# Kernel tuning notes

Hardware: AMD Instinct MI355X
Metric: run time of the kernel (lower is better)

Reference implementation:

```python
import jax, jax.numpy as jnp
import numpy as np

N_SITES = 16
BATCH = 8192
K = 256
EPS = 1e-10


def _entanglement_entropy(sites_A, sites_B):
    # sites_A: [b, pA, k], sites_B: [b, pB, k]
    corr = jnp.einsum('bik,bjk->bij', sites_A, sites_B)  # [b, pA, pB]
    s = jnp.linalg.svd(corr, compute_uv=False)           # [b, min(pA,pB)]
    s_sq = s * s + EPS
    p = s_sq / jnp.sum(s_sq, axis=-1, keepdims=True)
    return -jnp.sum(p * jnp.log(p + EPS), axis=-1)        # [b]


def setup_inputs() -> dict:
    key = jax.random.key(0)
    sites = jax.random.normal(key, (BATCH, N_SITES, K), dtype=jnp.float32)
    return {"sites": sites}


def reference(sites) -> jnp.ndarray:
    # sites: [batch, n_sites, k]; list-of-tensors in the original, stacked here.
    n = sites.shape[1]
    mid = n // 2  # 8
    # Whole-system bipartition
    S_whole = _entanglement_entropy(sites[:, :mid], sites[:, mid:])
    # Left half bipartition (mid_left = mid // 2 = 4)
    ml = mid // 2
    S_left = _entanglement_entropy(sites[:, :ml], sites[:, ml:mid])
    # Right half bipartition
    nr = n - mid
    mr = nr // 2
    S_right = _entanglement_entropy(sites[:, mid:mid + mr], sites[:, mid + mr:])
    phi_q = S_whole - (S_left + S_right)
    return jax.nn.relu(phi_q)
```

## Files before the change

### kernel.cpp

```cpp
#include <hip/hip_runtime.h>
#include <math.h>

#define DEV __device__ __forceinline__

typedef float v2f __attribute__((ext_vector_type(2)));

DEV float rcp_fast(float x) { return __builtin_amdgcn_rcpf(x); }
DEV float rsq_fast(float x) { return __builtin_amdgcn_rsqf(x); }

__host__ __device__ constexpr int TI(int n, int i, int j) {
  return n * i - (i * (i - 1)) / 2 + (j - i);
}

template <int N>
DEV float& sym_at(float (&a)[N * (N + 1) / 2], int i, int j) {
  return (i <= j) ? a[TI(N, i, j)] : a[TI(N, j, i)];
}

template <int N>
DEV void pivot_params(float (&a)[N * (N + 1) / 2], int p, int q,
                      float& c_out, float& s_out) {
  float apq = a[TI(N, p, q)];
  float app = a[TI(N, p, p)];
  float aqq = a[TI(N, q, q)];
  float h = aqq - app;
  float tw = apq + apq;
  float den = fabsf(h) + sqrtf(fmaf(h, h, tw * tw)) + 1e-37f;
  float t = tw * rcp_fast(den);
  t = (h < 0.0f) ? -t : t;
  float c = rsq_fast(fmaf(t, t, 1.0f));
  float s = t * c;
  c_out = c;
  s_out = s;
  a[TI(N, p, p)] = fmaf(-t, apq, app);
  a[TI(N, q, q)] = fmaf( t, apq, aqq);
  a[TI(N, p, q)] = 0.0f;
}

template <int N>
DEV void cross_update(float (&a)[N * (N + 1) / 2], int pa, int qa, int pb,
                      int qb, float ca, float sa, float cb, float sb) {
  float w = sym_at<N>(a, pa, pb), x = sym_at<N>(a, pa, qb);
  float y = sym_at<N>(a, qa, pb), z = sym_at<N>(a, qa, qb);
  float w1 = fmaf(ca, w, -sa * y), x1 = fmaf(ca, x, -sa * z);
  float y1 = fmaf(sa, w,  ca * y), z1 = fmaf(sa, x,  ca * z);
  sym_at<N>(a, pa, pb) = fmaf(cb, w1, -sb * x1);
  sym_at<N>(a, pa, qb) = fmaf(sb, w1,  cb * x1);
  sym_at<N>(a, qa, pb) = fmaf(cb, y1, -sb * z1);
  sym_at<N>(a, qa, qb) = fmaf(sb, y1,  cb * z1);
}

template <int SWEEPS>
DEV void pjacobi8(float (&a)[36]) {
  constexpr int P[7][4][2] = {
      {{0, 7}, {1, 6}, {2, 5}, {3, 4}}, {{0, 1}, {2, 7}, {3, 6}, {4, 5}},
      {{0, 2}, {1, 3}, {4, 7}, {5, 6}}, {{0, 3}, {2, 4}, {1, 5}, {6, 7}},
      {{0, 4}, {3, 5}, {2, 6}, {1, 7}}, {{0, 5}, {4, 6}, {3, 7}, {1, 2}},
      {{0, 6}, {5, 7}, {1, 4}, {2, 3}}};
  for (int sw = 0; sw < SWEEPS; ++sw) {
#pragma unroll
    for (int r = 0; r < 7; ++r) {
      float cc[4], ss[4];
#pragma unroll
      for (int u = 0; u < 4; ++u)
        pivot_params<8>(a, P[r][u][0], P[r][u][1], cc[u], ss[u]);
#pragma unroll
      for (int u = 0; u < 4; ++u) {
#pragma unroll
        for (int v = u + 1; v < 4; ++v) {
          cross_update<8>(a, P[r][u][0], P[r][u][1], P[r][v][0], P[r][v][1],
                          cc[u], ss[u], cc[v], ss[v]);
        }
      }
    }
  }
}

template <int SWEEPS>
DEV void pjacobi4x2(float (&a)[10], float (&b)[10]) {
  constexpr int P[3][2][2] = {
      {{0, 3}, {1, 2}}, {{0, 1}, {2, 3}}, {{0, 2}, {1, 3}}};
  for (int sw = 0; sw < SWEEPS; ++sw) {
#pragma unroll
    for (int r = 0; r < 3; ++r) {
      float ca0, sa0, ca1, sa1, cb0, sb0, cb1, sb1;
      pivot_params<4>(a, P[r][0][0], P[r][0][1], ca0, sa0);
      pivot_params<4>(b, P[r][0][0], P[r][0][1], cb0, sb0);
      pivot_params<4>(a, P[r][1][0], P[r][1][1], ca1, sa1);
      pivot_params<4>(b, P[r][1][0], P[r][1][1], cb1, sb1);
      cross_update<4>(a, P[r][0][0], P[r][0][1], P[r][1][0], P[r][1][1], ca0,
                      sa0, ca1, sa1);
      cross_update<4>(b, P[r][0][0], P[r][0][1], P[r][1][0], P[r][1][1], cb0,
                      sb0, cb1, sb1);
    }
  }
}

template <int N>
DEV float entropy_of(const float (&a)[N * (N + 1) / 2]) {
  float lam[N];
  float sum = 0.0f;
#pragma unroll
  for (int i = 0; i < N; ++i) {
    float l = fmaxf(a[TI(N, i, i)], 0.0f) + 1e-10f;
    lam[i] = l;
    sum += l;
  }
  float inv = 1.0f / sum;
  float H = 0.0f;
#pragma unroll
  for (int i = 0; i < N; ++i) {
    float p = lam[i] * inv;
    H = fmaf(p, __logf(p + 1e-10f), H);
  }
  return -H;
}

__global__ __launch_bounds__(256) void corr_kernel(
    const float* __restrict__ sites, float* __restrict__ cmat) {
  const int lane = threadIdx.x & 63;
  const int b = blockIdx.x * 4 + (threadIdx.x >> 6);
  const float4* base = reinterpret_cast<const float4*>(sites) + (size_t)b * 1024;

  v2f lo[16], hi[16];
#pragma unroll
  for (int s = 0; s < 16; ++s) {
    float4 f = base[s * 64 + lane];
    lo[s] = v2f{f.x, f.y};
    hi[s] = v2f{f.z, f.w};
  }

  const int up0 = lane & 1;

  float w[32];
#pragma unroll
  for (int m = 0; m < 32; ++m) {
    const int e0 = 2 * m, e1 = 2 * m + 1;
    const int i0 = e0 >> 3, j0 = e0 & 7;
    const int i1 = e1 >> 3, j1 = e1 & 7;
    v2f t0 = __builtin_elementwise_fma(hi[i0], hi[8 + j0], lo[i0] * lo[8 + j0]);
    v2f t1 = __builtin_elementwise_fma(hi[i1], hi[8 + j1], lo[i1] * lo[8 + j1]);
    float p0 = t0.x + t0.y;
    float p1 = t1.x + t1.y;
    float snd = up0 ? p0 : p1;
    float kp  = up0 ? p1 : p0;
    w[m] = kp + __shfl_xor(snd, 1, 64);
  }
#pragma unroll
  for (int d = 1; d < 6; ++d) {
    const int dist = 1 << d;
    const int up = (lane >> d) & 1;
#pragma unroll
    for (int m = 0; m < (64 >> (d + 1)); ++m) {
      float snd = up ? w[2 * m]     : w[2 * m + 1];
      float kp  = up ? w[2 * m + 1] : w[2 * m];
      w[m] = kp + __shfl_xor(snd, dist, 64);
    }
  }
  float cw = w[0];

  float x[16];
#pragma unroll
  for (int m = 0; m < 16; ++m) {
    const int e0 = 2 * m, e1 = 2 * m + 1;
    const int base_a = (e0 < 16) ? 0 : 8;
    const int ii0 = ((e0 & 15) >> 2), jj0 = (e0 & 3);
    const int ii1 = ((e1 & 15) >> 2), jj1 = (e1 & 3);
    v2f t0 = __builtin_elementwise_fma(hi[base_a + ii0], hi[base_a + 4 + jj0],
                                       lo[base_a + ii0] * lo[base_a + 4 + jj0]);
    v2f t1 = __builtin_elementwise_fma(hi[base_a + ii1], hi[base_a + 4 + jj1],
                                       lo[base_a + ii1] * lo[base_a + 4 + jj1]);
    float p0 = t0.x + t0.y;
    float p1 = t1.x + t1.y;
    float snd = up0 ? p0 : p1;
    float kp  = up0 ? p1 : p0;
    x[m] = kp + __shfl_xor(snd, 1, 64);
  }
#pragma unroll
  for (int d = 1; d < 5; ++d) {
    const int dist = 1 << d;
    const int up = (lane >> d) & 1;
#pragma unroll
    for (int m = 0; m < (32 >> (d + 1)); ++m) {
      float snd = up ? x[2 * m]     : x[2 * m + 1];
      float kp  = up ? x[2 * m + 1] : x[2 * m];
      x[m] = kp + __shfl_xor(snd, dist, 64);
    }
  }
  float clr = x[0] + __shfl_xor(x[0], 32, 64);

  float* row = cmat + (size_t)b * 96;
  row[lane] = cw;
  if (lane < 32) row[64 + lane] = clr;
}

__global__ __launch_bounds__(64) void phi_kernel(
    const float* __restrict__ cmat, float* __restrict__ out) {
  __shared__ float4 lds[64 * 25];
  const int t = threadIdx.x;
  const int b0 = blockIdx.x * 64;

  const float4* src = reinterpret_cast<const float4*>(cmat) + (size_t)b0 * 24;
#pragma unroll
  for (int r = 0; r < 24; ++r) {
    int q = r * 64 + t;
    float4 val = src[q];
    int bl = q / 24;
    int e4 = q - bl * 24;
    lds[bl * 25 + e4] = val;
  }
  __syncthreads();

  const float4* myrow = &lds[t * 25];
  float Cw[64], Cl[16], Cr[16];
#pragma unroll
  for (int j = 0; j < 16; ++j) {
    float4 f = myrow[j];
    Cw[4 * j] = f.x; Cw[4 * j + 1] = f.y; Cw[4 * j + 2] = f.z; Cw[4 * j + 3] = f.w;
  }
#pragma unroll
  for (int j = 0; j < 4; ++j) {
    float4 f = myrow[16 + j];
    Cl[4 * j] = f.x; Cl[4 * j + 1] = f.y; Cl[4 * j + 2] = f.z; Cl[4 * j + 3] = f.w;
    float4 g = myrow[20 + j];
    Cr[4 * j] = g.x; Cr[4 * j + 1] = g.y; Cr[4 * j + 2] = g.z; Cr[4 * j + 3] = g.w;
  }

  float Mw[36];
#pragma unroll
  for (int i = 0; i < 8; ++i) {
#pragma unroll
    for (int j = i; j < 8; ++j) {
      float acc = 0.0f;
#pragma unroll
      for (int k = 0; k < 8; ++k) acc = fmaf(Cw[i * 8 + k], Cw[j * 8 + k], acc);
      Mw[TI(8, i, j)] = acc;
    }
  }
  float Ml[10], Mr[10];
#pragma unroll
  for (int i = 0; i < 4; ++i) {
#pragma unroll
    for (int j = i; j < 4; ++j) {
      float accl = 0.0f, accr = 0.0f;
#pragma unroll
      for (int k = 0; k < 4; ++k) {
        accl = fmaf(Cl[i * 4 + k], Cl[j * 4 + k], accl);
        accr = fmaf(Cr[i * 4 + k], Cr[j * 4 + k], accr);
      }
      Ml[TI(4, i, j)] = accl;
      Mr[TI(4, i, j)] = accr;
    }
  }

  pjacobi8<3>(Mw);
  pjacobi4x2<3>(Ml, Mr);

  float Sw = entropy_of<8>(Mw);
  float Sl = entropy_of<4>(Ml);
  float Sr = entropy_of<4>(Mr);

  out[b0 + t] = fmaxf(Sw - Sl - Sr, 0.0f);
}

extern "C" void kernel_launch(void* const* d_in, const int* in_sizes, int n_in,
                              void* d_out, int out_size, void* d_ws, size_t ws_size,
                              hipStream_t stream) {
  const float* sites = (const float*)d_in[0];
  float* out = (float*)d_out;
  float* cmat = (float*)d_ws;

  corr_kernel<<<2048, 256, 0, stream>>>(sites, cmat);
  phi_kernel<<<128, 64, 0, stream>>>(cmat, out);
}
```

Baseline: 204.3 us.

## Fuse correlation and Jacobi entropy kernels into one launch via LDS

Merges the correlation kernel and the phi/Jacobi kernel into a single kernel. Each block writes its four batch rows of correlation values into shared memory, and then four threads run the Jacobi eigen-solve and entropy for those rows. This removes the workspace round trip through global memory and the second kernel launch. In exchange, the serial Jacobi work now runs on only four threads per 256-thread block while the other threads sit idle, and the same 256-register-class launch bounds now apply to the heavy solver code.

```diff
diff --git a/kernel.cpp b/kernel.cpp
--- a/kernel.cpp
+++ b/kernel.cpp
@@ -116,10 +116,12 @@
   return -H;
 }
 
-__global__ __launch_bounds__(256) void corr_kernel(
-    const float* __restrict__ sites, float* __restrict__ cmat) {
+__global__ __launch_bounds__(256) void phiq_fused(
+    const float* __restrict__ sites, float* __restrict__ out) {
+  __shared__ float lds[4 * 100];
   const int lane = threadIdx.x & 63;
-  const int b = blockIdx.x * 4 + (threadIdx.x >> 6);
+  const int w = threadIdx.x >> 6;
+  const int b = blockIdx.x * 4 + w;
   const float4* base = reinterpret_cast<const float4*>(sites) + (size_t)b * 1024;
 
   v2f lo[16], hi[16];
@@ -132,7 +134,7 @@
 
   const int up0 = lane & 1;
 
-  float w[32];
+  float wbuf[32];
 #pragma unroll
   for (int m = 0; m < 32; ++m) {
     const int e0 = 2 * m, e1 = 2 * m + 1;
@@ -144,7 +146,7 @@
     float p1 = t1.x + t1.y;
     float snd = up0 ? p0 : p1;
     float kp  = up0 ? p1 : p0;
-    w[m] = kp + __shfl_xor(snd, 1, 64);
+    wbuf[m] = kp + __shfl_xor(snd, 1, 64);
   }
 #pragma unroll
   for (int d = 1; d < 6; ++d) {
@@ -152,14 +154,14 @@
     const int up = (lane >> d) & 1;
 #pragma unroll
     for (int m = 0; m < (64 >> (d + 1)); ++m) {
-      float snd = up ? w[2 * m]     : w[2 * m + 1];
-      float kp  = up ? w[2 * m + 1] : w[2 * m];
-      w[m] = kp + __shfl_xor(snd, dist, 64);
-    }
-  }
-  float cw = w[0];
-
-  float x[16];
+      float snd = up ? wbuf[2 * m]     : wbuf[2 * m + 1];
+      float kp  = up ? wbuf[2 * m + 1] : wbuf[2 * m];
+      wbuf[m] = kp + __shfl_xor(snd, dist, 64);
+    }
+  }
+  float cw = wbuf[0];
+
+  float xbuf[16];
 #pragma unroll
   for (int m = 0; m < 16; ++m) {
     const int e0 = 2 * m, e1 = 2 * m + 1;
@@ -174,7 +176,7 @@
     float p1 = t1.x + t1.y;
     float snd = up0 ? p0 : p1;
     float kp  = up0 ? p1 : p0;
-    x[m] = kp + __shfl_xor(snd, 1, 64);
+    xbuf[m] = kp + __shfl_xor(snd, 1, 64);
   }
 #pragma unroll
   for (int d = 1; d < 5; ++d) {
@@ -182,36 +184,23 @@
     const int up = (lane >> d) & 1;
 #pragma unroll
     for (int m = 0; m < (32 >> (d + 1)); ++m) {
-      float snd = up ? x[2 * m]     : x[2 * m + 1];
-      float kp  = up ? x[2 * m + 1] : x[2 * m];
-      x[m] = kp + __shfl_xor(snd, dist, 64);
-    }
-  }
-  float clr = x[0] + __shfl_xor(x[0], 32, 64);
-
-  float* row = cmat + (size_t)b * 96;
+      float snd = up ? xbuf[2 * m]     : xbuf[2 * m + 1];
+      float kp  = up ? xbuf[2 * m + 1] : xbuf[2 * m];
+      xbuf[m] = kp + __shfl_xor(snd, dist, 64);
+    }
+  }
+  float clr = xbuf[0] + __shfl_xor(xbuf[0], 32, 64);
+
+  float* row = lds + w * 100;
   row[lane] = cw;
   if (lane < 32) row[64 + lane] = clr;
-}
-
-__global__ __launch_bounds__(64) void phi_kernel(
-    const float* __restrict__ cmat, float* __restrict__ out) {
-  __shared__ float4 lds[64 * 25];
+  __syncthreads();
+
+  if (threadIdx.x >= 4) return;
+
   const int t = threadIdx.x;
-  const int b0 = blockIdx.x * 64;
-
-  const float4* src = reinterpret_cast<const float4*>(cmat) + (size_t)b0 * 24;
-#pragma unroll
-  for (int r = 0; r < 24; ++r) {
-    int q = r * 64 + t;
-    float4 val = src[q];
-    int bl = q / 24;
-    int e4 = q - bl * 24;
-    lds[bl * 25 + e4] = val;
-  }
-  __syncthreads();
-
-  const float4* myrow = &lds[t * 25];
+  const float4* myrow = reinterpret_cast<const float4*>(lds + t * 100);
+
   float Cw[64], Cl[16], Cr[16];
 #pragma unroll
   for (int j = 0; j < 16; ++j) {
@@ -260,7 +249,7 @@
   float Sl = entropy_of<4>(Ml);
   float Sr = entropy_of<4>(Mr);
 
-  out[b0 + t] = fmaxf(Sw - Sl - Sr, 0.0f);
+  out[blockIdx.x * 4 + t] = fmaxf(Sw - Sl - Sr, 0.0f);
 }
 
 extern "C" void kernel_launch(void* const* d_in, const int* in_sizes, int n_in,
@@ -268,8 +257,7 @@
                               hipStream_t stream) {
   const float* sites = (const float*)d_in[0];
   float* out = (float*)d_out;
-  float* cmat = (float*)d_ws;
-
-  corr_kernel<<<2048, 256, 0, stream>>>(sites, cmat);
-  phi_kernel<<<128, 64, 0, stream>>>(cmat, out);
-}
+  (void)d_ws; (void)ws_size;
+
+  phiq_fused<<<2048, 256, 0, stream>>>(sites, out);
+}
```

Result: slower. 262.0 us (+28.2%).
